# Kernel tuning notes

Measured on AMD Instinct MI355X. Metric: run time of the kernel, lower is better.

Reference implementation:

```python
import jax, jax.numpy as jnp
import numpy as np

B = 8192      # batch
T = 8         # obs_len
E = 256       # feature_dim
M = 20        # num_modes
NH = 4        # attention heads
HD = E // NH  # head dim
FS = 12       # future_steps
LN_EPS = 1e-5


def setup_inputs() -> dict:
    key = jax.random.key(0)
    ks = jax.random.split(key, 32)
    s = 0.05
    def n(i, shape):
        return jax.random.normal(ks[i], shape, jnp.float32) * s
    return {
        "observed_trajectory": jax.random.normal(ks[0], (B, T, 2), jnp.float32),
        # 2-layer LSTM (torch gate order i,f,g,o)
        "w_ih0": n(1, (4 * E, 2)), "w_hh0": n(2, (4 * E, E)),
        "b_ih0": n(3, (4 * E,)), "b_hh0": n(4, (4 * E,)),
        "w_ih1": n(5, (4 * E, E)), "w_hh1": n(6, (4 * E, E)),
        "b_ih1": n(7, (4 * E,)), "b_hh1": n(8, (4 * E,)),
        # 20 MHA modules, weights stacked over mode axis
        "in_proj_w": n(9, (M, 3 * E, E)), "in_proj_b": n(10, (M, 3 * E)),
        "out_w": n(11, (M, E, E)), "out_b": n(12, (M, E)),
        # FFN: LN -> Linear(256,1024) -> ReLU -> Linear(1024,256) -> LN
        "ln1_g": jnp.ones((E,)), "ln1_b": jnp.zeros((E,)),
        "ffn_w1": n(13, (1024, E)), "ffn_b1": n(14, (1024,)),
        "ffn_w2": n(15, (E, 1024)), "ffn_b2": n(16, (E,)),
        "ln2_g": jnp.ones((E,)), "ln2_b": jnp.zeros((E,)),
        # decoder MLP
        "dec_w1": n(17, (512, E)), "dec_b1": n(18, (512,)),
        "dec_w2": n(19, (FS * 2, 512)), "dec_b2": n(20, (FS * 2,)),
        # scorer MLP
        "sc_w1": n(21, (128, E)), "sc_b1": n(22, (128,)),
        "sc_w2": n(23, (1, 128)), "sc_b2": n(24, (1,)),
    }


def _lstm_layer(xs, w_ih, w_hh, b_ih, b_hh):
    # xs: (T, B, in_dim) -> (ys (T,B,E), h_T (B,E))
    bb = xs.shape[1]
    h0 = jnp.zeros((bb, E), xs.dtype)
    c0 = jnp.zeros((bb, E), xs.dtype)
    def step(carry, x):
        h, c = carry
        g = x @ w_ih.T + h @ w_hh.T + b_ih + b_hh
        i, f, gg, o = jnp.split(g, 4, axis=-1)
        c = jax.nn.sigmoid(f) * c + jax.nn.sigmoid(i) * jnp.tanh(gg)
        h = jax.nn.sigmoid(o) * jnp.tanh(c)
        return (h, c), h
    (h_t, _), ys = jax.lax.scan(step, (h0, c0), xs)
    return ys, h_t


def _ln(x, g, b):
    m = jnp.mean(x, -1, keepdims=True)
    v = jnp.mean((x - m) ** 2, -1, keepdims=True)
    return (x - m) * jax.lax.rsqrt(v + LN_EPS) * g + b


def _forward(observed_trajectory, w_ih0, w_hh0, b_ih0, b_hh0,
             w_ih1, w_hh1, b_ih1, b_hh1,
             in_proj_w, in_proj_b, out_w, out_b,
             ln1_g, ln1_b, ffn_w1, ffn_b1, ffn_w2, ffn_b2, ln2_g, ln2_b,
             dec_w1, dec_b1, dec_w2, dec_b2,
             sc_w1, sc_b1, sc_w2, sc_b2):
    bsz = observed_trajectory.shape[0]
    # --- TrajectoryEncoder: 2-layer LSTM, take last-step output of layer 2 ---
    xs = jnp.transpose(observed_trajectory, (1, 0, 2))  # (T, B, 2)
    ys0, _ = _lstm_layer(xs, w_ih0, w_hh0, b_ih0, b_hh0)
    _, emb = _lstm_layer(ys0, w_ih1, w_hh1, b_ih1, b_hh1)  # (B, E)

    # --- MultiModalTransformer: 20 MHA modules on seq_len=1 (fused over modes) ---
    # query == key == value == emb. Dropout is eval-mode identity.
    qkv = jnp.einsum('be,mfe->bmf', emb, in_proj_w) + in_proj_b  # (B, M, 3E)
    q, k, v = jnp.split(qkv, 3, axis=-1)
    q = q.reshape(bsz, M, NH, HD)
    k = k.reshape(bsz, M, NH, HD)
    v = v.reshape(bsz, M, NH, HD)
    # kv length is 1 -> softmax over a single score is identically 1
    scores = jnp.sum(q * k, -1, keepdims=True) / jnp.sqrt(jnp.float32(HD))  # (B,M,NH,1)
    attn = jax.nn.softmax(scores, axis=-1)
    ctx = (attn * v).reshape(bsz, M, E)
    attn_out = jnp.einsum('bmf,mof->bmo', ctx, out_w) + out_b  # (B, M, E)
    # FFN (no residual in original module)
    h = _ln(attn_out, ln1_g, ln1_b)
    h = jax.nn.relu(h @ ffn_w1.T + ffn_b1)
    h = h @ ffn_w2.T + ffn_b2
    mm_emb = _ln(h, ln2_g, ln2_b)  # (B, M, E)

    # --- TrajectoryDecoder ---
    last_pos = observed_trajectory[:, -1, :]  # (B, 2)
    d = jax.nn.elu(mm_emb @ dec_w1.T + dec_b1)
    deltas = (d @ dec_w2.T + dec_b2).reshape(bsz, M, FS, 2)
    predictions = deltas + last_pos[:, None, None, :]

    # --- ModeScorer ---
    s = jax.nn.elu(mm_emb @ sc_w1.T + sc_b1)
    scores_out = (s @ sc_w2.T + sc_b2)[..., 0]  # (B, M)
    return predictions, scores_out


def reference(observed_trajectory, w_ih0, w_hh0, b_ih0, b_hh0,
              w_ih1, w_hh1, b_ih1, b_hh1,
              in_proj_w, in_proj_b, out_w, out_b,
              ln1_g, ln1_b, ffn_w1, ffn_b1, ffn_w2, ffn_b2, ln2_g, ln2_b,
              dec_w1, dec_b1, dec_w2, dec_b2,
              sc_w1, sc_b1, sc_w2, sc_b2):
    return _forward(observed_trajectory, w_ih0, w_hh0, b_ih0, b_hh0,
                    w_ih1, w_hh1, b_ih1, b_hh1,
                    in_proj_w, in_proj_b, out_w, out_b,
                    ln1_g, ln1_b, ffn_w1, ffn_b1, ffn_w2, ffn_b2, ln2_g, ln2_b,
                    dec_w1, dec_b1, dec_w2, dec_b2,
                    sc_w1, sc_b1, sc_w2, sc_b2)
```

## Files before the change

kernel.cpp:

```cpp
#include <hip/hip_runtime.h>
#include <math.h>


typedef float4 f4;
typedef unsigned int u32;
typedef unsigned short u16;
typedef __attribute__((ext_vector_type(16))) float f32x16;
typedef __attribute__((ext_vector_type(8)))  short s16x8;

__device__ __forceinline__ float sigm(float x){ return 1.0f/(1.0f + __expf(-x)); }
__device__ __forceinline__ float tanhfast(float x){ return 2.0f*sigm(2.0f*x) - 1.0f; }
__device__ __forceinline__ float eluf(float x){ return x > 0.f ? x : expm1f(x); }
__device__ __forceinline__ u16 f2bf(float x){
  u32 u = __float_as_uint(x);
  return (u16)((u + 0x7FFFu + ((u>>16)&1u)) >> 16);
}
__device__ __forceinline__ float bf2f(u16 h){ return __uint_as_float(((u32)h)<<16); }


#define LSTR 264

__global__ __launch_bounds__(256, 4)
void w2c_kernel(const float* __restrict__ out_w, const float* __restrict__ ipw,
                float* __restrict__ W2c)
{
  __shared__ float As[16][68];
  __shared__ float Bs2[16][68];
  const int tid = threadIdx.x;
  const int m = blockIdx.y;
  const int o0 = (blockIdx.x >> 2) * 64, e0 = (blockIdx.x & 3) * 64;
  const int trow = tid >> 4, tcol = tid & 15;
  const float* Ap = out_w + (size_t)m * 65536;
  const float* Bp = ipw + ((size_t)m * 768 + 512) * 256;
  float acc[16];
#pragma unroll
  for (int z = 0; z < 16; ++z) acc[z] = 0.f;
  for (int kb = 0; kb < 256; kb += 16) {
    { int row = tid >> 2, ko = (tid & 3) * 4;
      f4 v = *(const f4*)(Ap + (size_t)(o0+row)*256 + kb + ko);
      As[ko+0][row]=v.x; As[ko+1][row]=v.y; As[ko+2][row]=v.z; As[ko+3][row]=v.w; }
    { int k = tid >> 4, eo = (tid & 15) * 4;
      *(f4*)&Bs2[k][eo] = *(const f4*)(Bp + (size_t)(kb+k)*256 + e0 + eo); }
    __syncthreads();
#pragma unroll
    for (int k = 0; k < 16; ++k) {
      f4 a4 = *(const f4*)&As[k][trow*4];
      f4 b4 = *(const f4*)&Bs2[k][tcol*4];
      acc[0]+=a4.x*b4.x; acc[1]+=a4.x*b4.y; acc[2]+=a4.x*b4.z; acc[3]+=a4.x*b4.w;
      acc[4]+=a4.y*b4.x; acc[5]+=a4.y*b4.y; acc[6]+=a4.y*b4.z; acc[7]+=a4.y*b4.w;
      acc[8]+=a4.z*b4.x; acc[9]+=a4.z*b4.y; acc[10]+=a4.z*b4.z; acc[11]+=a4.z*b4.w;
      acc[12]+=a4.w*b4.x; acc[13]+=a4.w*b4.y; acc[14]+=a4.w*b4.z; acc[15]+=a4.w*b4.w;
    }
    __syncthreads();
  }
#pragma unroll
  for (int i = 0; i < 4; ++i)
    *(f4*)&W2c[((size_t)m*256 + o0 + trow*4 + i)*256 + e0 + tcol*4] =
        make_float4(acc[i*4+0], acc[i*4+1], acc[i*4+2], acc[i*4+3]);
}

__global__ void b2c_kernel(const float* __restrict__ out_w, const float* __restrict__ out_b,
                           const float* __restrict__ ipb, float* __restrict__ b2c)
{
  __shared__ float pb[256];
  const int m = blockIdx.x, o = threadIdx.x;
  pb[o] = ipb[(size_t)m*768 + 512 + o];
  __syncthreads();
  const float* wr = out_w + ((size_t)m*256 + o)*256;
  float acc = out_b[(size_t)m*256 + o];
  for (int f = 0; f < 256; f += 4) {
    f4 w = *(const f4*)&wr[f];
    acc += w.x*pb[f] + w.y*pb[f+1] + w.z*pb[f+2] + w.w*pb[f+3];
  }
  b2c[(size_t)m*256 + o] = acc;
}

__device__ __forceinline__ void cvt_seg(const float* __restrict__ src, u16* __restrict__ dst,
                                        int Creal, int lognks, int g)
{
  const int l = g & 63;
  const int cks = g >> 6;
  const int ks = cks & ((1 << lognks) - 1);
  const int ct = cks >> lognks;
  const int c = ct*32 + (l & 31);
  const int K = 16 << lognks;
  const int k = ks*16 + ((l >> 5) * 8);
  s16x8 r;
  if (c < Creal) {
    const float* s = src + (size_t)c * K + k;
    f4 v0 = *(const f4*)s;
    f4 v1 = *(const f4*)(s + 4);
    r[0]=(short)f2bf(v0.x); r[1]=(short)f2bf(v0.y); r[2]=(short)f2bf(v0.z); r[3]=(short)f2bf(v0.w);
    r[4]=(short)f2bf(v1.x); r[5]=(short)f2bf(v1.y); r[6]=(short)f2bf(v1.z); r[7]=(short)f2bf(v1.w);
  } else {
#pragma unroll
    for (int j = 0; j < 8; ++j) r[j] = 0;
  }
  *(s16x8*)(dst + (size_t)g * 8) = r;
}

__global__ __launch_bounds__(256)
void wcvt_all(const float* __restrict__ whh0, const float* __restrict__ wih1,
              const float* __restrict__ whh1, const float* __restrict__ W2c,
              const float* __restrict__ ffn1, const float* __restrict__ ffn2,
              const float* __restrict__ dec1, const float* __restrict__ dec2,
              const float* __restrict__ sc1,  u16* __restrict__ dst)
{
  int g = blockIdx.x * 256 + threadIdx.x;
  if      (g <  32768) cvt_seg(whh0, dst + 0,       1024, 4, g);
  else if (g <  65536) cvt_seg(wih1, dst + 262144,  1024, 4, g - 32768);
  else if (g <  98304) cvt_seg(whh1, dst + 524288,  1024, 4, g - 65536);
  else if (g < 262144) cvt_seg(W2c,  dst + 786432,  5120, 4, g - 98304);
  else if (g < 294912) cvt_seg(ffn1, dst + 2097152, 1024, 4, g - 262144);
  else if (g < 327680) cvt_seg(ffn2, dst + 2359296,  256, 6, g - 294912);
  else if (g < 344064) cvt_seg(dec1, dst + 2621440,  512, 4, g - 327680);
  else if (g < 346112) cvt_seg(dec2, dst + 2752512,   24, 5, g - 344064);
  else if (g < 350208) cvt_seg(sc1,  dst + 2768896,  128, 4, g - 346112);
}

__global__ __launch_bounds__(512, 2)
void lstm_fused(const u16* __restrict__ whh0f, const u16* __restrict__ wih1f,
                const u16* __restrict__ whh1f, const float* __restrict__ w_ih0,
                const float* __restrict__ b_ih0, const float* __restrict__ b_hh0,
                const float* __restrict__ b_ih1, const float* __restrict__ b_hh1,
                const float* __restrict__ obs, u16* __restrict__ emb)
{
  __shared__ u16 h0s[32 * LSTR];
  __shared__ u16 h1s[32 * LSTR];
  __shared__ float obs_s[512];
  const int tid = threadIdx.x;
  const int lane = tid & 63, w = tid >> 6;
  const int col = lane & 31, hi = lane >> 5;
  const int r0 = blockIdx.x * 32;
  if (tid < 512) obs_s[tid] = obs[(size_t)r0 * 16 + tid];

  float bs0[4], bs1[4], xw0[4], xw1[4];
#pragma unroll
  for (int g = 0; g < 4; ++g) {
    const int cg = g*256 + w*32 + col;
    bs0[g] = b_ih0[cg] + b_hh0[cg];
    bs1[g] = b_ih1[cg] + b_hh1[cg];
    xw0[g] = w_ih0[2*cg];
    xw1[g] = w_ih0[2*cg + 1];
  }
  float c0v[16], c1v[16];
#pragma unroll
  for (int r = 0; r < 16; ++r) { c0v[r] = 0.f; c1v[r] = 0.f; }

  f32x16 za;
#pragma unroll
  for (int i = 0; i < 16; ++i) za[i] = 0.f;

  __syncthreads();

  for (int t = 0; t < 8; ++t) {
    f32x16 accA[4], accB[4];
#pragma unroll
    for (int g = 0; g < 4; ++g) { accA[g] = za; accB[g] = za; }
    if (t > 0) {
#pragma unroll 2
      for (int ks = 0; ks < 16; ++ks) {
        s16x8 a0 = *(const s16x8*)(h0s + col*LSTR + ks*16 + hi*8);
        s16x8 a1 = *(const s16x8*)(h1s + col*LSTR + ks*16 + hi*8);
#pragma unroll
        for (int g = 0; g < 4; ++g) {
          const size_t fo = ((size_t)((g*8 + w)*16 + ks)*64 + lane)*8;
          s16x8 bA = *(const s16x8*)(whh0f + fo);
          accA[g] = __builtin_amdgcn_mfma_f32_32x32x16_bf16(a0, bA, accA[g], 0, 0, 0);
          s16x8 bB = *(const s16x8*)(whh1f + fo);
          accB[g] = __builtin_amdgcn_mfma_f32_32x32x16_bf16(a1, bB, accB[g], 0, 0, 0);
        }
      }
    }
    __syncthreads();
#pragma unroll
    for (int r = 0; r < 16; ++r) {
      const int row = (r&3) + 8*(r>>2) + 4*hi;
      const float x0 = obs_s[row*16 + 2*t], x1 = obs_s[row*16 + 2*t + 1];
      const float gi = accA[0][r] + bs0[0] + x0*xw0[0] + x1*xw1[0];
      const float gf = accA[1][r] + bs0[1] + x0*xw0[1] + x1*xw1[1];
      const float gg = accA[2][r] + bs0[2] + x0*xw0[2] + x1*xw1[2];
      const float go = accA[3][r] + bs0[3] + x0*xw0[3] + x1*xw1[3];
      const float cn = sigm(gf)*c0v[r] + sigm(gi)*tanhfast(gg);
      c0v[r] = cn;
      h0s[row*LSTR + w*32 + col] = f2bf(sigm(go)*tanhfast(cn));
    }
    __syncthreads();
#pragma unroll 4
    for (int ks = 0; ks < 16; ++ks) {
      s16x8 a = *(const s16x8*)(h0s + col*LSTR + ks*16 + hi*8);
#pragma unroll
      for (int g = 0; g < 4; ++g) {
        s16x8 b = *(const s16x8*)(wih1f + ((size_t)((g*8 + w)*16 + ks)*64 + lane)*8);
        accB[g] = __builtin_amdgcn_mfma_f32_32x32x16_bf16(a, b, accB[g], 0, 0, 0);
      }
    }
#pragma unroll
    for (int r = 0; r < 16; ++r) {
      const int row = (r&3) + 8*(r>>2) + 4*hi;
      const float gi = accB[0][r] + bs1[0];
      const float gf = accB[1][r] + bs1[1];
      const float gg = accB[2][r] + bs1[2];
      const float go = accB[3][r] + bs1[3];
      const float cn = sigm(gf)*c1v[r] + sigm(gi)*tanhfast(gg);
      c1v[r] = cn;
      h1s[row*LSTR + w*32 + col] = f2bf(sigm(go)*tanhfast(cn));
    }
    __syncthreads();
  }
#pragma unroll
  for (int kk = 0; kk < 2; ++kk) {
    const int gi2 = tid + kk*512;
    const int row = gi2 >> 5, grp = gi2 & 31;
    *(s16x8*)(emb + (size_t)(r0 + row)*256 + grp*8) = *(const s16x8*)(h1s + row*LSTR + grp*8);
  }
}

__device__ __forceinline__ void gemm128(const u16* As, const u16* __restrict__ Bf,
                                        f32x16 acc[2], int ct, int rh, int lane)
{
  const int col = lane & 31, hi = lane >> 5;
#pragma unroll 4
  for (int ks = 0; ks < 16; ++ks) {
    s16x8 b = *(const s16x8*)(Bf + ((size_t)(ct*16 + ks)*64 + lane)*8);
#pragma unroll
    for (int i = 0; i < 2; ++i) {
      s16x8 a = *(const s16x8*)(As + ((rh*2 + i)*32 + col)*LSTR + ks*16 + hi*8);
      acc[i] = __builtin_amdgcn_mfma_f32_32x32x16_bf16(a, b, acc[i], 0, 0, 0);
    }
  }
}

__device__ __forceinline__ void gemm_ffn2_128(const u16* As, const u16* __restrict__ Bf,
                                              f32x16 acc[2], int c4, int ct, int rh, int lane)
{
  const int col = lane & 31, hi = lane >> 5;
#pragma unroll 4
  for (int ks = 0; ks < 16; ++ks) {
    s16x8 b = *(const s16x8*)(Bf + ((size_t)(ct*64 + c4*16 + ks)*64 + lane)*8);
#pragma unroll
    for (int i = 0; i < 2; ++i) {
      s16x8 a = *(const s16x8*)(As + ((rh*2 + i)*32 + col)*LSTR + ks*16 + hi*8);
      acc[i] = __builtin_amdgcn_mfma_f32_32x32x16_bf16(a, b, acc[i], 0, 0, 0);
    }
  }
}

template<int ACT>
__device__ __forceinline__ void epi_store128(f32x16 acc[2], const float* __restrict__ bias,
                                             u16* Ys, int ct, int rh, int lane)
{
  const int col = lane & 31, hi = lane >> 5, cg = ct*32 + col;
  const float bv = bias[cg];
#pragma unroll
  for (int i = 0; i < 2; ++i)
#pragma unroll
    for (int r = 0; r < 16; ++r) {
      float v = acc[i][r] + bv;
      if (ACT == 1) v = fmaxf(v, 0.f);
      else if (ACT == 2) v = eluf(v);
      const int row = (rh*2 + i)*32 + (r&3) + 8*(r>>2) + 4*hi;
      Ys[row*LSTR + cg] = f2bf(v);
    }
}

__device__ __forceinline__ void lnpass128(const u16* In, u16* Out,
    const float* __restrict__ g, const float* __restrict__ b, int tid)
{
  const int lane = tid & 63, w = tid >> 6;
  f4 gv = *(const f4*)&g[lane*4];
  f4 bv = *(const f4*)&b[lane*4];
#pragma unroll
  for (int i = 0; i < 8; ++i) {
    const int row = w*8 + i;
    ushort4 uv = *(const ushort4*)(In + row*LSTR + lane*4);
    float v0 = bf2f(uv.x), v1 = bf2f(uv.y), v2 = bf2f(uv.z), v3 = bf2f(uv.w);
    float s  = v0 + v1 + v2 + v3;
    float ss = v0*v0 + v1*v1 + v2*v2 + v3*v3;
#pragma unroll
    for (int d = 1; d < 64; d <<= 1) { s += __shfl_xor(s, d); ss += __shfl_xor(ss, d); }
    const float mean = s * (1.f/256.f);
    const float rs = rsqrtf(ss * (1.f/256.f) - mean*mean + 1e-5f);
    ushort4 o;
    o.x = f2bf((v0 - mean)*rs*gv.x + bv.x);
    o.y = f2bf((v1 - mean)*rs*gv.y + bv.y);
    o.z = f2bf((v2 - mean)*rs*gv.z + bv.z);
    o.w = f2bf((v3 - mean)*rs*gv.w + bv.w);
    *(ushort4*)(Out + row*LSTR + lane*4) = o;
  }
}

__global__ __launch_bounds__(1024, 4)
void mode_stack(const u16* __restrict__ emb, const u16* __restrict__ W2cf,
  const float* __restrict__ b2c,
  const float* __restrict__ ln1_g, const float* __restrict__ ln1_b,
  const u16* __restrict__ ffn1f, const float* __restrict__ ffn_b1,
  const u16* __restrict__ ffn2f, const float* __restrict__ ffn_b2,
  const float* __restrict__ ln2_g, const float* __restrict__ ln2_b,
  const u16* __restrict__ dec1f, const float* __restrict__ dec_b1,
  const u16* __restrict__ dec2f, const float* __restrict__ dec_b2,
  const u16* __restrict__ sc1f,  const float* __restrict__ sc_b1,
  const float* __restrict__ sc_w2, const float* __restrict__ sc_b2,
  const float* __restrict__ obs, float* __restrict__ pred, float* __restrict__ score)
{
  __shared__ u16 Xs[128 * LSTR];
  __shared__ u16 Ys[128 * LSTR];
  __shared__ float obs_ls[256];
  const int tid = threadIdx.x;
  const int lane = tid & 63, w = tid >> 6;
  const int ct = w & 7, rh = w >> 3;
  const int col = lane & 31, hi = lane >> 5;
  const int r0 = blockIdx.x * 128;
  const int m  = blockIdx.y;

  f32x16 za;
#pragma unroll
  for (int i = 0; i < 16; ++i) za[i] = 0.f;

#pragma unroll
  for (int kk = 0; kk < 4; ++kk) {
    const int gi2 = tid + kk*1024;
    const int row = gi2 >> 5, grp = gi2 & 31;
    *(s16x8*)(Xs + row*LSTR + grp*8) = *(const s16x8*)(emb + (size_t)(r0 + row)*256 + grp*8);
  }
  if (tid < 256) obs_ls[tid] = obs[(size_t)(r0 + (tid >> 1))*16 + 14 + (tid & 1)];
  __syncthreads();

  {
    f32x16 acc[2]; acc[0] = za; acc[1] = za;
    gemm128(Xs, W2cf + (size_t)m*65536, acc, ct, rh, lane);
    epi_store128<0>(acc, b2c + m*256, Ys, ct, rh, lane);
  }
  __syncthreads();
  lnpass128(Ys, Xs, ln1_g, ln1_b, tid);
  __syncthreads();

  f32x16 h2[2]; h2[0] = za; h2[1] = za;
  for (int c4 = 0; c4 < 4; ++c4) {
    f32x16 tacc[2]; tacc[0] = za; tacc[1] = za;
    gemm128(Xs, ffn1f + (size_t)c4*65536, tacc, ct, rh, lane);
    epi_store128<1>(tacc, ffn_b1 + c4*256, Ys, ct, rh, lane);
    __syncthreads();
    gemm_ffn2_128(Ys, ffn2f, h2, c4, ct, rh, lane);
    __syncthreads();
  }
  epi_store128<0>(h2, ffn_b2, Ys, ct, rh, lane);
  __syncthreads();
  lnpass128(Ys, Xs, ln2_g, ln2_b, tid);
  __syncthreads();

  f32x16 dv[2]; dv[0] = za; dv[1] = za;
  for (int c2 = 0; c2 < 2; ++c2) {
    f32x16 tacc[2]; tacc[0] = za; tacc[1] = za;
    gemm128(Xs, dec1f + (size_t)c2*65536, tacc, ct, rh, lane);
    epi_store128<2>(tacc, dec_b1 + c2*256, Ys, ct, rh, lane);
    __syncthreads();
    if (ct == 0) {
#pragma unroll 4
      for (int ks = 0; ks < 16; ++ks) {
        s16x8 b = *(const s16x8*)(dec2f + ((size_t)(c2*16 + ks)*64 + lane)*8);
#pragma unroll
        for (int i = 0; i < 2; ++i) {
          s16x8 a = *(const s16x8*)(Ys + ((rh*2 + i)*32 + col)*LSTR + ks*16 + hi*8);
          dv[i] = __builtin_amdgcn_mfma_f32_32x32x16_bf16(a, b, dv[i], 0, 0, 0);
        }
      }
    }
    __syncthreads();
  }
  if (ct == 0 && col < 24) {
    const float db = dec_b2[col];
#pragma unroll
    for (int i = 0; i < 2; ++i)
#pragma unroll
      for (int r = 0; r < 16; ++r) {
        const int row = (rh*2 + i)*32 + (r&3) + 8*(r>>2) + 4*hi;
        const float lp = obs_ls[row*2 + (col & 1)];
        pred[((size_t)(r0 + row)*20 + m)*24 + col] = dv[i][r] + db + lp;
      }
  }

  if (ct < 4) {
    f32x16 sacc[2]; sacc[0] = za; sacc[1] = za;
    gemm128(Xs, sc1f, sacc, ct, rh, lane);
    epi_store128<2>(sacc, sc_b1, Ys, ct, rh, lane);
  }
  __syncthreads();
  {
    const float scb2 = sc_b2[0];
    const float2 w2v = *(const float2*)&sc_w2[lane*2];
#pragma unroll
    for (int i = 0; i < 8; ++i) {
      const int row = w*8 + i;
      u32 pv = *(const u32*)(Ys + row*LSTR + lane*2);
      float part = bf2f((u16)(pv & 0xFFFF))*w2v.x + bf2f((u16)(pv >> 16))*w2v.y;
#pragma unroll
      for (int d = 1; d < 64; d <<= 1) part += __shfl_xor(part, d);
      if (lane == 0) score[(size_t)(r0 + row)*20 + m] = part + scb2;
    }
  }
}

extern "C" void kernel_launch(void* const* d_in, const int* in_sizes, int n_in,
                              void* d_out, int out_size, void* d_ws, size_t ws_size,
                              hipStream_t stream)
{
  (void)in_sizes; (void)n_in; (void)out_size; (void)ws_size;
  const float* obs    = (const float*)d_in[0];
  const float* w_ih0  = (const float*)d_in[1];
  const float* w_hh0  = (const float*)d_in[2];
  const float* b_ih0  = (const float*)d_in[3];
  const float* b_hh0  = (const float*)d_in[4];
  const float* w_ih1  = (const float*)d_in[5];
  const float* w_hh1  = (const float*)d_in[6];
  const float* b_ih1  = (const float*)d_in[7];
  const float* b_hh1  = (const float*)d_in[8];
  const float* ipw    = (const float*)d_in[9];
  const float* ipb    = (const float*)d_in[10];
  const float* out_w  = (const float*)d_in[11];
  const float* out_b  = (const float*)d_in[12];
  const float* ln1_g  = (const float*)d_in[13];
  const float* ln1_b  = (const float*)d_in[14];
  const float* ffn_w1 = (const float*)d_in[15];
  const float* ffn_b1 = (const float*)d_in[16];
  const float* ffn_w2 = (const float*)d_in[17];
  const float* ffn_b2 = (const float*)d_in[18];
  const float* ln2_g  = (const float*)d_in[19];
  const float* ln2_b  = (const float*)d_in[20];
  const float* dec_w1 = (const float*)d_in[21];
  const float* dec_b1 = (const float*)d_in[22];
  const float* dec_w2 = (const float*)d_in[23];
  const float* dec_b2 = (const float*)d_in[24];
  const float* sc_w1  = (const float*)d_in[25];
  const float* sc_b1  = (const float*)d_in[26];
  const float* sc_w2  = (const float*)d_in[27];
  const float* sc_b2  = (const float*)d_in[28];

  float* outp   = (float*)d_out;
  float* pred   = outp;
  float* scoreo = outp + (size_t)8192*20*24;

  float* wsf   = (float*)d_ws;
  float* W2c   = wsf;
  float* b2cp  = wsf + 1310720;
  u16*   wsh   = (u16*)(wsf + 1315840);
  u16* whh0f = wsh + 0;
  u16* wih1f = wsh + 262144;
  u16* whh1f = wsh + 524288;
  u16* W2cf  = wsh + 786432;
  u16* ffn1f = wsh + 2097152;
  u16* ffn2f = wsh + 2359296;
  u16* dec1f = wsh + 2621440;
  u16* dec2f = wsh + 2752512;
  u16* sc1f  = wsh + 2768896;
  u16* emb   = wsh + 2801664;

  w2c_kernel<<<dim3(16, 20), 256, 0, stream>>>(out_w, ipw, W2c);
  b2c_kernel<<<20, 256, 0, stream>>>(out_w, out_b, ipb, b2cp);
  wcvt_all<<<1368, 256, 0, stream>>>(w_hh0, w_ih1, w_hh1, W2c, ffn_w1, ffn_w2,
                                     dec_w1, dec_w2, sc_w1, wsh);
  lstm_fused<<<256, 512, 0, stream>>>(whh0f, wih1f, whh1f, w_ih0, b_ih0, b_hh0,
                                      b_ih1, b_hh1, obs, emb);
  mode_stack<<<dim3(64, 20), 1024, 0, stream>>>(emb, W2cf, b2cp,
      ln1_g, ln1_b, ffn1f, ffn_b1, ffn2f, ffn_b2, ln2_g, ln2_b,
      dec1f, dec_b1, dec2f, dec_b2, sc1f, sc_b1, sc_w2, sc_b2,
      obs, pred, scoreo);
}
```

Baseline: 811.3 us.

## Skew LSTM layers across timesteps and halve mode_stack tile rows

The LSTM now computes layer-0 step 0 in a prologue. Each loop iteration then does layer-1 step t and layer-0 step t+1 together, reading the same h0 fragment for both GEMMs, which removes one barrier and one separate GEMM phase per timestep. mode_stack moves from 128-row, 1024-thread blocks to 64-row, 512-thread blocks, doubling the grid and halving shared memory per block to raise occupancy. The change also wraps the MFMA loops in s_setprio and replaces expm1f in ELU with __expf(x)-1. That ELU form loses some accuracy for small negative inputs.

```diff
diff --git a/kernel.cpp b/kernel.cpp
--- a/kernel.cpp
+++ b/kernel.cpp
@@ -10,7 +10,7 @@
 
 __device__ __forceinline__ float sigm(float x){ return 1.0f/(1.0f + __expf(-x)); }
 __device__ __forceinline__ float tanhfast(float x){ return 2.0f*sigm(2.0f*x) - 1.0f; }
-__device__ __forceinline__ float eluf(float x){ return x > 0.f ? x : expm1f(x); }
+__device__ __forceinline__ float eluf(float x){ return x > 0.f ? x : __expf(x) - 1.0f; }
 __device__ __forceinline__ u16 f2bf(float x){
   u32 u = __float_as_uint(x);
   return (u16)((u + 0x7FFFu + ((u>>16)&1u)) >> 16);
@@ -132,7 +132,7 @@
   const int lane = tid & 63, w = tid >> 6;
   const int col = lane & 31, hi = lane >> 5;
   const int r0 = blockIdx.x * 32;
-  if (tid < 512) obs_s[tid] = obs[(size_t)r0 * 16 + tid];
+  obs_s[tid] = obs[(size_t)r0 * 16 + tid];
 
   float bs0[4], bs1[4], xw0[4], xw1[4];
 #pragma unroll
@@ -152,11 +152,23 @@
   for (int i = 0; i < 16; ++i) za[i] = 0.f;
 
   __syncthreads();
+#pragma unroll
+  for (int r = 0; r < 16; ++r) {
+    const int row = (r&3) + 8*(r>>2) + 4*hi;
+    const float x0 = obs_s[row*16], x1 = obs_s[row*16 + 1];
+    const float gi = bs0[0] + x0*xw0[0] + x1*xw1[0];
+    const float gg = bs0[2] + x0*xw0[2] + x1*xw1[2];
+    const float go = bs0[3] + x0*xw0[3] + x1*xw1[3];
+    const float cn = sigm(gi)*tanhfast(gg);
+    c0v[r] = cn;
+    h0s[row*LSTR + w*32 + col] = f2bf(sigm(go)*tanhfast(cn));
+  }
+  __syncthreads();
 
   for (int t = 0; t < 8; ++t) {
-    f32x16 accA[4], accB[4];
-#pragma unroll
-    for (int g = 0; g < 4; ++g) { accA[g] = za; accB[g] = za; }
+    f32x16 aL1[4], aL0[4];
+#pragma unroll
+    for (int g = 0; g < 4; ++g) { aL1[g] = za; aL0[g] = za; }
     if (t > 0) {
 #pragma unroll 2
       for (int ks = 0; ks < 16; ++ks) {
@@ -165,46 +177,53 @@
 #pragma unroll
         for (int g = 0; g < 4; ++g) {
           const size_t fo = ((size_t)((g*8 + w)*16 + ks)*64 + lane)*8;
-          s16x8 bA = *(const s16x8*)(whh0f + fo);
-          accA[g] = __builtin_amdgcn_mfma_f32_32x32x16_bf16(a0, bA, accA[g], 0, 0, 0);
-          s16x8 bB = *(const s16x8*)(whh1f + fo);
-          accB[g] = __builtin_amdgcn_mfma_f32_32x32x16_bf16(a1, bB, accB[g], 0, 0, 0);
+          s16x8 b0 = *(const s16x8*)(wih1f + fo);
+          aL1[g] = __builtin_amdgcn_mfma_f32_32x32x16_bf16(a0, b0, aL1[g], 0, 0, 0);
+          s16x8 b1 = *(const s16x8*)(whh1f + fo);
+          aL1[g] = __builtin_amdgcn_mfma_f32_32x32x16_bf16(a1, b1, aL1[g], 0, 0, 0);
+          s16x8 b2 = *(const s16x8*)(whh0f + fo);
+          aL0[g] = __builtin_amdgcn_mfma_f32_32x32x16_bf16(a0, b2, aL0[g], 0, 0, 0);
         }
       }
+    } else {
+#pragma unroll 2
+      for (int ks = 0; ks < 16; ++ks) {
+        s16x8 a0 = *(const s16x8*)(h0s + col*LSTR + ks*16 + hi*8);
+#pragma unroll
+        for (int g = 0; g < 4; ++g) {
+          const size_t fo = ((size_t)((g*8 + w)*16 + ks)*64 + lane)*8;
+          s16x8 b0 = *(const s16x8*)(wih1f + fo);
+          aL1[g] = __builtin_amdgcn_mfma_f32_32x32x16_bf16(a0, b0, aL1[g], 0, 0, 0);
+          s16x8 b2 = *(const s16x8*)(whh0f + fo);
+          aL0[g] = __builtin_amdgcn_mfma_f32_32x32x16_bf16(a0, b2, aL0[g], 0, 0, 0);
+        }
+      }
     }
     __syncthreads();
 #pragma unroll
     for (int r = 0; r < 16; ++r) {
       const int row = (r&3) + 8*(r>>2) + 4*hi;
-      const float x0 = obs_s[row*16 + 2*t], x1 = obs_s[row*16 + 2*t + 1];
-      const float gi = accA[0][r] + bs0[0] + x0*xw0[0] + x1*xw1[0];
-      const float gf = accA[1][r] + bs0[1] + x0*xw0[1] + x1*xw1[1];
-      const float gg = accA[2][r] + bs0[2] + x0*xw0[2] + x1*xw1[2];
-      const float go = accA[3][r] + bs0[3] + x0*xw0[3] + x1*xw1[3];
-      const float cn = sigm(gf)*c0v[r] + sigm(gi)*tanhfast(gg);
-      c0v[r] = cn;
-      h0s[row*LSTR + w*32 + col] = f2bf(sigm(go)*tanhfast(cn));
-    }
-    __syncthreads();
-#pragma unroll 4
-    for (int ks = 0; ks < 16; ++ks) {
-      s16x8 a = *(const s16x8*)(h0s + col*LSTR + ks*16 + hi*8);
-#pragma unroll
-      for (int g = 0; g < 4; ++g) {
-        s16x8 b = *(const s16x8*)(wih1f + ((size_t)((g*8 + w)*16 + ks)*64 + lane)*8);
-        accB[g] = __builtin_amdgcn_mfma_f32_32x32x16_bf16(a, b, accB[g], 0, 0, 0);
-      }
-    }
-#pragma unroll
-    for (int r = 0; r < 16; ++r) {
-      const int row = (r&3) + 8*(r>>2) + 4*hi;
-      const float gi = accB[0][r] + bs1[0];
-      const float gf = accB[1][r] + bs1[1];
-      const float gg = accB[2][r] + bs1[2];
-      const float go = accB[3][r] + bs1[3];
+      const float gi = aL1[0][r] + bs1[0];
+      const float gf = aL1[1][r] + bs1[1];
+      const float gg = aL1[2][r] + bs1[2];
+      const float go = aL1[3][r] + bs1[3];
       const float cn = sigm(gf)*c1v[r] + sigm(gi)*tanhfast(gg);
       c1v[r] = cn;
       h1s[row*LSTR + w*32 + col] = f2bf(sigm(go)*tanhfast(cn));
+    }
+    if (t < 7) {
+#pragma unroll
+      for (int r = 0; r < 16; ++r) {
+        const int row = (r&3) + 8*(r>>2) + 4*hi;
+        const float x0 = obs_s[row*16 + 2*(t+1)], x1 = obs_s[row*16 + 2*(t+1) + 1];
+        const float gi = aL0[0][r] + bs0[0] + x0*xw0[0] + x1*xw1[0];
+        const float gf = aL0[1][r] + bs0[1] + x0*xw0[1] + x1*xw1[1];
+        const float gg = aL0[2][r] + bs0[2] + x0*xw0[2] + x1*xw1[2];
+        const float go = aL0[3][r] + bs0[3] + x0*xw0[3] + x1*xw1[3];
+        const float cn = sigm(gf)*c0v[r] + sigm(gi)*tanhfast(gg);
+        c0v[r] = cn;
+        h0s[row*LSTR + w*32 + col] = f2bf(sigm(go)*tanhfast(cn));
+      }
     }
     __syncthreads();
   }
@@ -216,39 +235,43 @@
   }
 }
 
-__device__ __forceinline__ void gemm128(const u16* As, const u16* __restrict__ Bf,
-                                        f32x16 acc[2], int ct, int rh, int lane)
+__device__ __forceinline__ void gemmP(const u16* As, const u16* __restrict__ Bf,
+                                      f32x16 acc[2], int ct, int lane)
 {
   const int col = lane & 31, hi = lane >> 5;
+  __builtin_amdgcn_s_setprio(1);
 #pragma unroll 4
   for (int ks = 0; ks < 16; ++ks) {
     s16x8 b = *(const s16x8*)(Bf + ((size_t)(ct*16 + ks)*64 + lane)*8);
 #pragma unroll
     for (int i = 0; i < 2; ++i) {
-      s16x8 a = *(const s16x8*)(As + ((rh*2 + i)*32 + col)*LSTR + ks*16 + hi*8);
+      s16x8 a = *(const s16x8*)(As + (i*32 + col)*LSTR + ks*16 + hi*8);
       acc[i] = __builtin_amdgcn_mfma_f32_32x32x16_bf16(a, b, acc[i], 0, 0, 0);
     }
   }
-}
-
-__device__ __forceinline__ void gemm_ffn2_128(const u16* As, const u16* __restrict__ Bf,
-                                              f32x16 acc[2], int c4, int ct, int rh, int lane)
+  __builtin_amdgcn_s_setprio(0);
+}
+
+__device__ __forceinline__ void gemmF2(const u16* As, const u16* __restrict__ Bf,
+                                       f32x16 acc[2], int c4, int ct, int lane)
 {
   const int col = lane & 31, hi = lane >> 5;
+  __builtin_amdgcn_s_setprio(1);
 #pragma unroll 4
   for (int ks = 0; ks < 16; ++ks) {
     s16x8 b = *(const s16x8*)(Bf + ((size_t)(ct*64 + c4*16 + ks)*64 + lane)*8);
 #pragma unroll
     for (int i = 0; i < 2; ++i) {
-      s16x8 a = *(const s16x8*)(As + ((rh*2 + i)*32 + col)*LSTR + ks*16 + hi*8);
+      s16x8 a = *(const s16x8*)(As + (i*32 + col)*LSTR + ks*16 + hi*8);
       acc[i] = __builtin_amdgcn_mfma_f32_32x32x16_bf16(a, b, acc[i], 0, 0, 0);
     }
   }
+  __builtin_amdgcn_s_setprio(0);
 }
 
 template<int ACT>
-__device__ __forceinline__ void epi_store128(f32x16 acc[2], const float* __restrict__ bias,
-                                             u16* Ys, int ct, int rh, int lane)
+__device__ __forceinline__ void epiP(f32x16 acc[2], const float* __restrict__ bias,
+                                     u16* Ys, int ct, int lane)
 {
   const int col = lane & 31, hi = lane >> 5, cg = ct*32 + col;
   const float bv = bias[cg];
@@ -259,12 +282,12 @@
       float v = acc[i][r] + bv;
       if (ACT == 1) v = fmaxf(v, 0.f);
       else if (ACT == 2) v = eluf(v);
-      const int row = (rh*2 + i)*32 + (r&3) + 8*(r>>2) + 4*hi;
+      const int row = i*32 + (r&3) + 8*(r>>2) + 4*hi;
       Ys[row*LSTR + cg] = f2bf(v);
     }
 }
 
-__device__ __forceinline__ void lnpass128(const u16* In, u16* Out,
+__device__ __forceinline__ void lnp(const u16* In, u16* Out,
     const float* __restrict__ g, const float* __restrict__ b, int tid)
 {
   const int lane = tid & 63, w = tid >> 6;
@@ -290,7 +313,7 @@
   }
 }
 
-__global__ __launch_bounds__(1024, 4)
+__global__ __launch_bounds__(512, 4)
 void mode_stack(const u16* __restrict__ emb, const u16* __restrict__ W2cf,
   const float* __restrict__ b2c,
   const float* __restrict__ ln1_g, const float* __restrict__ ln1_b,
@@ -303,14 +326,14 @@
   const float* __restrict__ sc_w2, const float* __restrict__ sc_b2,
   const float* __restrict__ obs, float* __restrict__ pred, float* __restrict__ score)
 {
-  __shared__ u16 Xs[128 * LSTR];
-  __shared__ u16 Ys[128 * LSTR];
-  __shared__ float obs_ls[256];
+  __shared__ u16 Xs[64 * LSTR];
+  __shared__ u16 Ys[64 * LSTR];
+  __shared__ float obs_ls[128];
   const int tid = threadIdx.x;
   const int lane = tid & 63, w = tid >> 6;
-  const int ct = w & 7, rh = w >> 3;
+  const int ct = w;
   const int col = lane & 31, hi = lane >> 5;
-  const int r0 = blockIdx.x * 128;
+  const int r0 = blockIdx.x * 64;
   const int m  = blockIdx.y;
 
   f32x16 za;
@@ -319,71 +342,71 @@
 
 #pragma unroll
   for (int kk = 0; kk < 4; ++kk) {
-    const int gi2 = tid + kk*1024;
+    const int gi2 = tid + kk*512;
     const int row = gi2 >> 5, grp = gi2 & 31;
     *(s16x8*)(Xs + row*LSTR + grp*8) = *(const s16x8*)(emb + (size_t)(r0 + row)*256 + grp*8);
   }
-  if (tid < 256) obs_ls[tid] = obs[(size_t)(r0 + (tid >> 1))*16 + 14 + (tid & 1)];
+  if (tid < 128) obs_ls[tid] = obs[(size_t)(r0 + (tid >> 1))*16 + 14 + (tid & 1)];
   __syncthreads();
 
   {
     f32x16 acc[2]; acc[0] = za; acc[1] = za;
-    gemm128(Xs, W2cf + (size_t)m*65536, acc, ct, rh, lane);
-    epi_store128<0>(acc, b2c + m*256, Ys, ct, rh, lane);
-  }
-  __syncthreads();
-  lnpass128(Ys, Xs, ln1_g, ln1_b, tid);
+    gemmP(Xs, W2cf + (size_t)m*65536, acc, ct, lane);
+    epiP<0>(acc, b2c + m*256, Ys, ct, lane);
+  }
+  __syncthreads();
+  lnp(Ys, Xs, ln1_g, ln1_b, tid);
   __syncthreads();
 
   f32x16 h2[2]; h2[0] = za; h2[1] = za;
   for (int c4 = 0; c4 < 4; ++c4) {
     f32x16 tacc[2]; tacc[0] = za; tacc[1] = za;
-    gemm128(Xs, ffn1f + (size_t)c4*65536, tacc, ct, rh, lane);
-    epi_store128<1>(tacc, ffn_b1 + c4*256, Ys, ct, rh, lane);
-    __syncthreads();
-    gemm_ffn2_128(Ys, ffn2f, h2, c4, ct, rh, lane);
-    __syncthreads();
-  }
-  epi_store128<0>(h2, ffn_b2, Ys, ct, rh, lane);
-  __syncthreads();
-  lnpass128(Ys, Xs, ln2_g, ln2_b, tid);
+    gemmP(Xs, ffn1f + (size_t)c4*65536, tacc, ct, lane);
+    epiP<1>(tacc, ffn_b1 + c4*256, Ys, ct, lane);
+    __syncthreads();
+    gemmF2(Ys, ffn2f, h2, c4, ct, lane);
+    __syncthreads();
+  }
+  epiP<0>(h2, ffn_b2, Ys, ct, lane);
+  __syncthreads();
+  lnp(Ys, Xs, ln2_g, ln2_b, tid);
   __syncthreads();
 
   f32x16 dv[2]; dv[0] = za; dv[1] = za;
   for (int c2 = 0; c2 < 2; ++c2) {
     f32x16 tacc[2]; tacc[0] = za; tacc[1] = za;
-    gemm128(Xs, dec1f + (size_t)c2*65536, tacc, ct, rh, lane);
-    epi_store128<2>(tacc, dec_b1 + c2*256, Ys, ct, rh, lane);
-    __syncthreads();
-    if (ct == 0) {
+    gemmP(Xs, dec1f + (size_t)c2*65536, tacc, ct, lane);
+    epiP<2>(tacc, dec_b1 + c2*256, Ys, ct, lane);
+    __syncthreads();
+    if (w == 0) {
 #pragma unroll 4
       for (int ks = 0; ks < 16; ++ks) {
         s16x8 b = *(const s16x8*)(dec2f + ((size_t)(c2*16 + ks)*64 + lane)*8);
 #pragma unroll
         for (int i = 0; i < 2; ++i) {
-          s16x8 a = *(const s16x8*)(Ys + ((rh*2 + i)*32 + col)*LSTR + ks*16 + hi*8);
+          s16x8 a = *(const s16x8*)(Ys + (i*32 + col)*LSTR + ks*16 + hi*8);
           dv[i] = __builtin_amdgcn_mfma_f32_32x32x16_bf16(a, b, dv[i], 0, 0, 0);
         }
       }
     }
     __syncthreads();
   }
-  if (ct == 0 && col < 24) {
+  if (w == 0 && col < 24) {
     const float db = dec_b2[col];
 #pragma unroll
     for (int i = 0; i < 2; ++i)
 #pragma unroll
       for (int r = 0; r < 16; ++r) {
-        const int row = (rh*2 + i)*32 + (r&3) + 8*(r>>2) + 4*hi;
+        const int row = i*32 + (r&3) + 8*(r>>2) + 4*hi;
         const float lp = obs_ls[row*2 + (col & 1)];
         pred[((size_t)(r0 + row)*20 + m)*24 + col] = dv[i][r] + db + lp;
       }
   }
 
-  if (ct < 4) {
+  if (w < 4) {
     f32x16 sacc[2]; sacc[0] = za; sacc[1] = za;
-    gemm128(Xs, sc1f, sacc, ct, rh, lane);
-    epi_store128<2>(sacc, sc_b1, Ys, ct, rh, lane);
+    gemmP(Xs, sc1f, sacc, ct, lane);
+    epiP<2>(sacc, sc_b1, Ys, ct, lane);
   }
   __syncthreads();
   {
@@ -461,7 +484,7 @@
                                      dec_w1, dec_w2, sc_w1, wsh);
   lstm_fused<<<256, 512, 0, stream>>>(whh0f, wih1f, whh1f, w_ih0, b_ih0, b_hh0,
                                       b_ih1, b_hh1, obs, emb);
-  mode_stack<<<dim3(64, 20), 1024, 0, stream>>>(emb, W2cf, b2cp,
+  mode_stack<<<dim3(128, 20), 512, 0, stream>>>(emb, W2cf, b2cp,
       ln1_g, ln1_b, ffn1f, ffn_b1, ffn2f, ffn_b2, ln2_g, ln2_b,
       dec1f, dec_b1, dec2f, dec_b2, sc1f, sc_b1, sc_w2, sc_b2,
       obs, pred, scoreo);
```

New measurement: 776.2 us. -4.3%, faster.
